# Performance work log

Hardware: AMD Instinct MI355X
Metric: run time of the kernel (lower is better)

## Reference

```python
import jax, jax.numpy as jnp
import numpy as np

B, S, D, H = 2, 2048, 1024, 16
DK = D // H


def setup_inputs() -> dict:
    key = jax.random.key(0)
    ks = jax.random.split(key, 11)
    sd = 1.0 / np.sqrt(D)  # torch Linear default init scale (uniform bound)
    def lin(k):
        kw, kb = jax.random.split(k)
        W = jax.random.uniform(kw, (D, D), jnp.float32, -sd, sd)
        b = jax.random.uniform(kb, (D,), jnp.float32, -sd, sd)
        return W, b
    Wq, bq = lin(ks[0]); Wk, bk = lin(ks[1]); Wv, bv = lin(ks[2]); Wo, bo = lin(ks[3])
    return {
        "Q": jax.random.normal(ks[4], (B, S, D), jnp.float32),
        "K": jax.random.normal(ks[5], (B, S, D), jnp.float32),
        "V": jax.random.normal(ks[6], (B, S, D), jnp.float32),
        "mask": jnp.ones((B, S), jnp.int32),
        "Wq": Wq, "bq": bq, "Wk": Wk, "bk": bk,
        "Wv": Wv, "bv": bv, "Wo": Wo, "bo": bo,
    }


def reference(Q, K, V, mask, Wq, bq, Wk, bk, Wv, bv, Wo, bo):
    b, s, _ = Q.shape
    # projections (torch Linear: x @ W.T + b), split heads -> [b, h, s, dk]
    def proj(x, W, bias):
        return (x @ W.T + bias).reshape(b, -1, H, DK).transpose(0, 2, 1, 3)
    q = proj(Q, Wq, bq)
    k = proj(K, Wk, bk)
    v = proj(V, Wv, bv)
    scores = jnp.einsum('bhqd,bhkd->bhqk', q, k) / jnp.sqrt(jnp.float32(DK))
    m = mask[:, None, None, :]  # [b,1,1,s_k]
    scores = jnp.where(m == 0, jnp.float32(-jnp.inf), scores)
    attn = jax.nn.softmax(scores, axis=-1)
    out = jnp.einsum('bhqk,bhkd->bhqd', attn, v)
    out = out.transpose(0, 2, 1, 3).reshape(b, s, H * DK)
    return out @ Wo.T + bo
```

## Files before the change

kernel.cpp:

```cpp
#include <hip/hip_runtime.h>
#include <stdint.h>

#define BB 2
#define HH 16
#define SS 2048
#define DKK 64
#define DD 1024
#define TT (BB * SS)

typedef __attribute__((ext_vector_type(8))) short bf16x8;
typedef __attribute__((ext_vector_type(4))) float f32x4;
typedef __attribute__((ext_vector_type(16))) float f32x16;

static __device__ __forceinline__ unsigned short f2bf(float f) {
  union { float f; uint32_t u; } c; c.f = f;
  return (unsigned short)((c.u + 0x7FFFu + ((c.u >> 16) & 1u)) >> 16);
}

static __device__ __forceinline__ f32x4 zero4() {
  f32x4 z; z[0] = 0.f; z[1] = 0.f; z[2] = 0.f; z[3] = 0.f; return z;
}
static __device__ __forceinline__ f32x16 zero16() {
  f32x16 z;
#pragma unroll
  for (int i = 0; i < 16; ++i) z[i] = 0.f;
  return z;
}

static __device__ __forceinline__ uint32_t cvt_pk_bf16(float lo, float hi) {
  uint32_t r;
  asm("v_cvt_pk_bf16_f32 %0, %1, %2" : "=v"(r) : "v"(lo), "v"(hi));
  return r;
}

static __device__ __forceinline__ uint32_t xswap_u32(uint32_t v) {
  return (uint32_t)__shfl_xor((int)v, 32);
}
static __device__ __forceinline__ float xhalf_sum(float x) {
  return x + __shfl_xor(x, 32);
}

static __device__ __forceinline__ void gload_lds16(const void* g, void* l) {
  __builtin_amdgcn_global_load_lds(
      (const __attribute__((address_space(1))) void*)g,
      (__attribute__((address_space(3))) void*)l, 16, 0, 0);
}

static __device__ __forceinline__ int swz(int row, int col) {
  return ((((col >> 3) ^ row) & 7) << 3) | (col & 7);
}

struct CvtArgs {
  const float* src[7];
  unsigned short* dst[7];
  int n4[7];
};

__global__ __launch_bounds__(256) void cvt_all(CvtArgs a) {
  const int id = blockIdx.y;
  const float4* s = (const float4*)a.src[id];
  ushort4* d = (ushort4*)a.dst[id];
  const int n4 = a.n4[id];
  for (int i = blockIdx.x * blockDim.x + threadIdx.x; i < n4;
       i += gridDim.x * blockDim.x) {
    float4 v = s[i];
    ushort4 o;
    o.x = f2bf(v.x); o.y = f2bf(v.y); o.z = f2bf(v.z); o.w = f2bf(v.w);
    d[i] = o;
  }
}

struct GemmJob {
  const unsigned short* A;
  const unsigned short* W;
  const float* bias;
  void* out;
  int mode;
  float scale;
};
struct GemmArgs { GemmJob job[3]; };

template <int BM, int NBUF>
__global__ __launch_bounds__(256) void gemm_kernel(GemmArgs args) {
  constexpr int MI = BM / 32;
  __shared__ __align__(16) unsigned short As[NBUF][BM][64];
  __shared__ __align__(16) unsigned short Bs[NBUF][128][64];
  const GemmJob jb = args.job[blockIdx.z];
  const int tid = threadIdx.x;
  const int lane = tid & 63;
  const int wv = tid >> 6;
  const int fr = lane & 15, fq = lane >> 4;
  const int wr = (wv >> 1) * (BM / 2), wc = (wv & 1) * 64;

  const int nb = gridDim.x * gridDim.y;
  const int bid = blockIdx.y * gridDim.x + blockIdx.x;
  const int virt = (bid & 7) * (nb >> 3) + (bid >> 3);
  const int n0 = (virt & 7) * 128, m0 = (virt >> 3) * BM;

  const int lrow = lane >> 3;
  const int lchunk = (lane & 7) ^ lrow;
  const unsigned short* __restrict__ A = jb.A;
  const unsigned short* __restrict__ W = jb.W;

  f32x4 acc[MI][4];
#pragma unroll
  for (int i = 0; i < MI; ++i)
#pragma unroll
    for (int j = 0; j < 4; ++j) acc[i][j] = zero4();

  constexpr int SEGA_W = BM / 32;
  constexpr int NT = DD / 64;

#define GSTAGE(buf, k0)                                                      \
  {                                                                          \
    _Pragma("unroll") for (int i = 0; i < SEGA_W; ++i) {                     \
      const int seg = wv * SEGA_W + i;                                       \
      const int row = seg * 8 + lrow;                                        \
      gload_lds16(A + (size_t)(m0 + row) * DD + (k0) + lchunk * 8,           \
                  (char*)&As[buf][0][0] + seg * 1024);                       \
    }                                                                        \
    _Pragma("unroll") for (int i = 0; i < 4; ++i) {                          \
      const int seg = wv * 4 + i;                                            \
      const int row = seg * 8 + lrow;                                        \
      gload_lds16(W + (size_t)(n0 + row) * DD + (k0) + lchunk * 8,           \
                  (char*)&Bs[buf][0][0] + seg * 1024);                       \
    }                                                                        \
  }

  int cur = 0;
  if (NBUF == 2) GSTAGE(0, 0);

  for (int t = 0; t < NT; ++t) {
    if (NBUF == 1) {
      __syncthreads();
      GSTAGE(0, t * 64);
      __syncthreads();
    } else {
      __syncthreads();
      if (t + 1 < NT) GSTAGE(cur ^ 1, (t + 1) * 64);
    }
#pragma unroll
    for (int kk = 0; kk < 2; ++kk) {
      bf16x8 af[MI], bfr[4];
#pragma unroll
      for (int i = 0; i < MI; ++i) {
        const int r = wr + i * 16 + fr;
        af[i] = *(const bf16x8*)&As[cur][r][swz(r, kk * 32 + fq * 8)];
      }
#pragma unroll
      for (int j = 0; j < 4; ++j) {
        const int r = wc + j * 16 + fr;
        bfr[j] = *(const bf16x8*)&Bs[cur][r][swz(r, kk * 32 + fq * 8)];
      }
      __builtin_amdgcn_s_setprio(1);
#pragma unroll
      for (int i = 0; i < MI; ++i)
#pragma unroll
        for (int j = 0; j < 4; ++j)
          acc[i][j] = __builtin_amdgcn_mfma_f32_16x16x32_bf16(af[i], bfr[j],
                                                              acc[i][j], 0, 0, 0);
      __builtin_amdgcn_s_setprio(0);
    }
    if (NBUF == 2) cur ^= 1;
  }
#undef GSTAGE

  const int mode = jb.mode;
  const float scale = jb.scale;
  if (mode == 1) {
    float* out = (float*)jb.out;
#pragma unroll
    for (int i = 0; i < MI; ++i)
#pragma unroll
      for (int j = 0; j < 4; ++j) {
        const int col = n0 + wc + j * 16 + fr;
        const float bv = jb.bias[col];
#pragma unroll
        for (int r = 0; r < 4; ++r) {
          const int row = m0 + wr + i * 16 + fq * 4 + r;
          out[(size_t)row * DD + col] = (acc[i][j][r] + bv) * scale;
        }
      }
  } else if (mode == 0) {
    unsigned short* out = (unsigned short*)jb.out;
#pragma unroll
    for (int i = 0; i < MI; ++i)
#pragma unroll
      for (int j = 0; j < 4; ++j) {
        const int col = n0 + wc + j * 16 + fr;
        const float bv = jb.bias[col];
        const int h = col >> 6, dk = col & 63;
#pragma unroll
        for (int r = 0; r < 4; ++r) {
          const int row = m0 + wr + i * 16 + fq * 4 + r;
          const int b = row >> 11, s = row & (SS - 1);
          out[(((size_t)(b * HH + h)) * SS + s) * DKK + dk] =
              f2bf((acc[i][j][r] + bv) * scale);
        }
      }
  } else {
    unsigned short* out = (unsigned short*)jb.out;
#pragma unroll
    for (int i = 0; i < MI; ++i)
#pragma unroll
      for (int j = 0; j < 4; ++j) {
        const int col = n0 + wc + j * 16 + fr;
        const float bv = jb.bias[col];
        const int h = col >> 6, dk = col & 63;
#pragma unroll
        for (int r = 0; r < 4; ++r) {
          const int row = m0 + wr + i * 16 + fq * 4 + r;
          const int b = row >> 11, s = row & (SS - 1);
          out[(((size_t)(b * HH + h)) * DKK + dk) * SS + s] =
              f2bf((acc[i][j][r] + bv) * scale);
        }
      }
  }
}

__global__ __launch_bounds__(512, 2) void attn_kernel(
    const unsigned short* __restrict__ qh, const unsigned short* __restrict__ kh,
    const unsigned short* __restrict__ vt, const int* __restrict__ maskp,
    unsigned short* __restrict__ ao) {
  __shared__ __align__(16) char smem[65536];

  const int tid = threadIdx.x;
  const int lane = tid & 63, wv = tid >> 6;
  const int lo = lane & 31, hi = lane >> 5;
  const int g = wv >> 2, qw = wv & 3;

  const int bid = blockIdx.x;
  const int virt = (bid & 7) * 32 + (bid >> 3);
  const int bh = virt >> 3, qblk = virt & 7;
  const int bB = bh >> 4, h = bh & 15;
  const int q0 = qblk * 256;
  const size_t base = (size_t)bh * SS * DKK;
  const size_t vbase = (size_t)bh * DKK * SS;

  const int lrow = lane >> 3;
  const int lchunk = (lane & 7) ^ lrow;
  const int srow = wv * 8 + lrow;

  bf16x8 aq[2][4];
#pragma unroll
  for (int st = 0; st < 2; ++st) {
    const int qrow = q0 + qw * 64 + st * 32 + lo;
#pragma unroll
    for (int tt = 0; tt < 4; ++tt)
      aq[st][tt] =
          *(const bf16x8*)(qh + base + (size_t)qrow * DKK + 16 * tt + hi * 8);
  }

  float lsum[2] = {0.f, 0.f};
  f32x16 o[2][2];
#pragma unroll
  for (int st = 0; st < 2; ++st) {
    o[st][0] = zero16();
    o[st][1] = zero16();
  }

  const int kvb = g * (SS / 2);
  constexpr int NTH = SS / 128;

  uint32_t okbits = 0;
  for (int t = 0; t < NTH; ++t) {
    const int mv = maskp[bB * SS + kvb + t * 64 + lane];
    okbits |= (__all(mv != 0)) ? (1u << t) : 0u;
  }

#define STAGE(d, t)                                                           \
  {                                                                           \
    const int ka = (t) * 64, kb2 = SS / 2 + (t) * 64;                         \
    gload_lds16(kh + base + (size_t)(ka + srow) * DKK + lchunk * 8,           \
                smem + ((d)) * 8192 + wv * 1024);                             \
    gload_lds16(vt + vbase + (size_t)srow * SS + ka + lchunk * 8,             \
                smem + 32768 + ((d)) * 8192 + wv * 1024);                     \
    gload_lds16(kh + base + (size_t)(kb2 + srow) * DKK + lchunk * 8,          \
                smem + (2 + (d)) * 8192 + wv * 1024);                         \
    gload_lds16(vt + vbase + (size_t)srow * SS + kb2 + lchunk * 8,            \
                smem + 32768 + (2 + (d)) * 8192 + wv * 1024);                 \
  }

  STAGE(0, 0);
  int cur = 0;

  for (int t = 0; t < NTH; ++t) {
    __syncthreads();
    if (t + 1 < NTH) STAGE(cur ^ 1, t + 1);
    const bool ok = (okbits >> t) & 1;

    const unsigned short* Ksb =
        (const unsigned short*)(smem + (g * 2 + cur) * 8192);
    const unsigned short* Vsb =
        (const unsigned short*)(smem + 32768 + (g * 2 + cur) * 8192);

    f32x16 sc[2][2];
#pragma unroll
    for (int st = 0; st < 2; ++st) { sc[st][0] = zero16(); sc[st][1] = zero16(); }
    __builtin_amdgcn_s_setprio(1);
#pragma unroll
    for (int tt = 0; tt < 4; ++tt) {
      bf16x8 k0 = *(const bf16x8*)&Ksb[lo * 64 + swz(lo, (hi + 2 * tt) * 8)];
      bf16x8 k1 =
          *(const bf16x8*)&Ksb[(32 + lo) * 64 + swz(32 + lo, (hi + 2 * tt) * 8)];
#pragma unroll
      for (int st = 0; st < 2; ++st) {
        sc[st][0] =
            __builtin_amdgcn_mfma_f32_32x32x16_bf16(k0, aq[st][tt], sc[st][0], 0, 0, 0);
        sc[st][1] =
            __builtin_amdgcn_mfma_f32_32x32x16_bf16(k1, aq[st][tt], sc[st][1], 0, 0, 0);
      }
    }
    __builtin_amdgcn_s_setprio(0);

    if (!ok) {
      const int mt = maskp[bB * SS + kvb + t * 64 + lane];
#pragma unroll
      for (int r = 0; r < 16; ++r) {
        const int kvi = (r & 3) + 8 * (r >> 2) + 4 * hi;
        const float a0 = (__shfl(mt, kvi) != 0) ? 0.f : -1e30f;
        const float a1 = (__shfl(mt, 32 + kvi) != 0) ? 0.f : -1e30f;
#pragma unroll
        for (int st = 0; st < 2; ++st) {
          sc[st][0][r] += a0;
          sc[st][1][r] += a1;
        }
      }
    }

    bf16x8 pb[2][4];
#pragma unroll
    for (int st = 0; st < 2; ++st) {
#pragma unroll
      for (int r = 0; r < 16; ++r) {
        sc[st][0][r] = __builtin_amdgcn_exp2f(sc[st][0][r]);
        sc[st][1][r] = __builtin_amdgcn_exp2f(sc[st][1][r]);
      }
      float t8[8];
#pragma unroll
      for (int i = 0; i < 8; ++i)
        t8[i] = (sc[st][0][2 * i] + sc[st][0][2 * i + 1]) +
                (sc[st][1][2 * i] + sc[st][1][2 * i + 1]);
      lsum[st] += ((t8[0] + t8[1]) + (t8[2] + t8[3])) +
                  ((t8[4] + t8[5]) + (t8[6] + t8[7]));

#pragma unroll
      for (int kb = 0; kb < 2; ++kb) {
#pragma unroll
        for (int tt = 0; tt < 2; ++tt) {
          const int b = tt * 8;
          uint32_t a0 = cvt_pk_bf16(sc[st][kb][b + 0], sc[st][kb][b + 1]);
          uint32_t a1 = cvt_pk_bf16(sc[st][kb][b + 2], sc[st][kb][b + 3]);
          uint32_t a2 = cvt_pk_bf16(sc[st][kb][b + 4], sc[st][kb][b + 5]);
          uint32_t a3 = cvt_pk_bf16(sc[st][kb][b + 6], sc[st][kb][b + 7]);
          const uint32_t e0 = xswap_u32(hi ? a0 : a2);
          const uint32_t e1 = xswap_u32(hi ? a1 : a3);
          union { uint32_t w[4]; bf16x8 v; } u;
          u.w[0] = hi ? e0 : a0;
          u.w[1] = hi ? e1 : a1;
          u.w[2] = hi ? a2 : e0;
          u.w[3] = hi ? a3 : e1;
          pb[st][kb * 2 + tt] = u.v;
        }
      }
    }

    __builtin_amdgcn_s_setprio(1);
#pragma unroll
    for (int tt = 0; tt < 4; ++tt) {
      bf16x8 v0 = *(const bf16x8*)&Vsb[lo * 64 + swz(lo, (hi + 2 * tt) * 8)];
      bf16x8 v1 =
          *(const bf16x8*)&Vsb[(32 + lo) * 64 + swz(32 + lo, (hi + 2 * tt) * 8)];
#pragma unroll
      for (int st = 0; st < 2; ++st) {
        o[st][0] = __builtin_amdgcn_mfma_f32_32x32x16_bf16(v0, pb[st][tt], o[st][0], 0, 0, 0);
        o[st][1] = __builtin_amdgcn_mfma_f32_32x32x16_bf16(v1, pb[st][tt], o[st][1], 0, 0, 0);
      }
    }
    __builtin_amdgcn_s_setprio(0);

    cur ^= 1;
  }
#undef STAGE

  lsum[0] = xhalf_sum(lsum[0]);
  lsum[1] = xhalf_sum(lsum[1]);

  float* mb = (float*)smem;
#pragma unroll
  for (int st = 0; st < 2; ++st) {
    const int rec = (qw * 64 + lane) * 33;
    __syncthreads();
    if (g == 1) {
      mb[rec] = lsum[st];
#pragma unroll
      for (int i = 0; i < 16; ++i) {
        mb[rec + 1 + i] = o[st][0][i];
        mb[rec + 17 + i] = o[st][1][i];
      }
    }
    __syncthreads();
    if (g == 0) {
      const float inv = 1.f / (lsum[st] + mb[rec]);
      const int token = bB * SS + q0 + qw * 64 + st * 32 + lo;
      unsigned short* aop = ao + (size_t)token * DD + h * DKK;
#pragma unroll
      for (int db = 0; db < 2; ++db) {
#pragma unroll
        for (int gq = 0; gq < 4; ++gq) {
          const int rb = rec + 1 + db * 16 + 4 * gq;
          float c0 = (o[st][db][4 * gq + 0] + mb[rb + 0]) * inv;
          float c1 = (o[st][db][4 * gq + 1] + mb[rb + 1]) * inv;
          float c2 = (o[st][db][4 * gq + 2] + mb[rb + 2]) * inv;
          float c3 = (o[st][db][4 * gq + 3] + mb[rb + 3]) * inv;
          uint2 w;
          w.x = cvt_pk_bf16(c0, c1);
          w.y = cvt_pk_bf16(c2, c3);
          *(uint2*)&aop[db * 32 + 8 * gq + 4 * hi] = w;
        }
      }
    }
  }
}

extern "C" void kernel_launch(void* const* d_in, const int* in_sizes, int n_in,
                              void* d_out, int out_size, void* d_ws, size_t ws_size,
                              hipStream_t stream) {
  const float* Q = (const float*)d_in[0];
  const float* K = (const float*)d_in[1];
  const float* V = (const float*)d_in[2];
  const int* mask = (const int*)d_in[3];
  const float* Wq = (const float*)d_in[4];
  const float* bq = (const float*)d_in[5];
  const float* Wk = (const float*)d_in[6];
  const float* bk = (const float*)d_in[7];
  const float* Wv = (const float*)d_in[8];
  const float* bv = (const float*)d_in[9];
  const float* Wo = (const float*)d_in[10];
  const float* bo = (const float*)d_in[11];

  char* ws = (char*)d_ws;
  const size_t SZ_X = (size_t)TT * DD * 2;
  const size_t SZ_W = (size_t)DD * DD * 2;
  unsigned short* Qb = (unsigned short*)(ws + 0 * SZ_X);
  unsigned short* Kb = (unsigned short*)(ws + 1 * SZ_X);
  unsigned short* Vb = (unsigned short*)(ws + 2 * SZ_X);
  unsigned short* Wqb = (unsigned short*)(ws + 3 * SZ_X);
  unsigned short* Wkb = (unsigned short*)(ws + 3 * SZ_X + 1 * SZ_W);
  unsigned short* Wvb = (unsigned short*)(ws + 3 * SZ_X + 2 * SZ_W);
  unsigned short* Wob = (unsigned short*)(ws + 3 * SZ_X + 3 * SZ_W);
  unsigned short* qh = (unsigned short*)(ws + 3 * SZ_X + 4 * SZ_W);
  unsigned short* kh = (unsigned short*)(ws + 4 * SZ_X + 4 * SZ_W);
  unsigned short* vt = (unsigned short*)(ws + 5 * SZ_X + 4 * SZ_W);
  unsigned short* ao = (unsigned short*)(ws + 6 * SZ_X + 4 * SZ_W);

  CvtArgs ca;
  ca.src[0] = Q;  ca.dst[0] = Qb;  ca.n4[0] = TT * DD / 4;
  ca.src[1] = K;  ca.dst[1] = Kb;  ca.n4[1] = TT * DD / 4;
  ca.src[2] = V;  ca.dst[2] = Vb;  ca.n4[2] = TT * DD / 4;
  ca.src[3] = Wq; ca.dst[3] = Wqb; ca.n4[3] = DD * DD / 4;
  ca.src[4] = Wk; ca.dst[4] = Wkb; ca.n4[4] = DD * DD / 4;
  ca.src[5] = Wv; ca.dst[5] = Wvb; ca.n4[5] = DD * DD / 4;
  ca.src[6] = Wo; ca.dst[6] = Wob; ca.n4[6] = DD * DD / 4;
  cvt_all<<<dim3(1024, 7), 256, 0, stream>>>(ca);

  const float SCALE_Q = 0.125f * 1.44269504088896f;

  GemmArgs ga;
  ga.job[0] = {Qb, Wqb, bq, qh, 0, SCALE_Q};
  ga.job[1] = {Kb, Wkb, bk, kh, 0, 1.0f};
  ga.job[2] = {Vb, Wvb, bv, vt, 2, 1.0f};
  gemm_kernel<64, 2><<<dim3(DD / 128, TT / 64, 3), 256, 0, stream>>>(ga);

  attn_kernel<<<dim3((TT / 256) * HH), 512, 0, stream>>>(qh, kh, vt, mask, ao);

  GemmArgs gf;
  gf.job[0] = {ao, Wob, bo, d_out, 1, 1.0f};
  gf.job[1] = gf.job[0];
  gf.job[2] = gf.job[0];
  gemm_kernel<64, 2><<<dim3(DD / 128, TT / 64, 1), 256, 0, stream>>>(gf);
}
```

Before: 113.5 us.

## Fuse fp32-to-bf16 activation conversion into QKV projection GEMM A-tile loads

The separate conversion pass for Q, K, V activations is removed; the QKV GEMM now reads fp32 activations directly, converts them to bf16 in registers and writes them to LDS, while weights are still pre-converted. This cuts the extra write and re-read of three bf16 activation copies (about 48MB of traffic) and shrinks the conversion kernel to weights only. In exchange, A-tile loads go through registers with synchronous global loads instead of async global-to-LDS copies, which may expose more latency in the GEMM main loop and doubles the A-side bytes read per tile.

```diff
diff --git a/kernel.cpp b/kernel.cpp
--- a/kernel.cpp
+++ b/kernel.cpp
@@ -51,9 +51,9 @@
 }
 
 struct CvtArgs {
-  const float* src[7];
-  unsigned short* dst[7];
-  int n4[7];
+  const float* src[4];
+  unsigned short* dst[4];
+  int n4[4];
 };
 
 __global__ __launch_bounds__(256) void cvt_all(CvtArgs a) {
@@ -71,7 +71,7 @@
 }
 
 struct GemmJob {
-  const unsigned short* A;
+  const void* A;
   const unsigned short* W;
   const float* bias;
   void* out;
@@ -80,7 +80,7 @@
 };
 struct GemmArgs { GemmJob job[3]; };
 
-template <int BM, int NBUF>
+template <int BM, int NBUF, bool AFP32>
 __global__ __launch_bounds__(256) void gemm_kernel(GemmArgs args) {
   constexpr int MI = BM / 32;
   __shared__ __align__(16) unsigned short As[NBUF][BM][64];
@@ -99,7 +99,8 @@
 
   const int lrow = lane >> 3;
   const int lchunk = (lane & 7) ^ lrow;
-  const unsigned short* __restrict__ A = jb.A;
+  const unsigned short* __restrict__ Ab = (const unsigned short*)jb.A;
+  const float* __restrict__ A32 = (const float*)jb.A;
   const unsigned short* __restrict__ W = jb.W;
 
   f32x4 acc[MI][4];
@@ -116,8 +117,20 @@
     _Pragma("unroll") for (int i = 0; i < SEGA_W; ++i) {                     \
       const int seg = wv * SEGA_W + i;                                       \
       const int row = seg * 8 + lrow;                                        \
-      gload_lds16(A + (size_t)(m0 + row) * DD + (k0) + lchunk * 8,           \
-                  (char*)&As[buf][0][0] + seg * 1024);                       \
+      if constexpr (AFP32) {                                                 \
+        const float* sp = A32 + (size_t)(m0 + row) * DD + (k0) + lchunk * 8; \
+        const float4 f0 = *(const float4*)sp;                                \
+        const float4 f1 = *(const float4*)(sp + 4);                          \
+        uint4 wdat;                                                          \
+        wdat.x = cvt_pk_bf16(f0.x, f0.y);                                    \
+        wdat.y = cvt_pk_bf16(f0.z, f0.w);                                    \
+        wdat.z = cvt_pk_bf16(f1.x, f1.y);                                    \
+        wdat.w = cvt_pk_bf16(f1.z, f1.w);                                    \
+        *(uint4*)((char*)&As[buf][0][0] + seg * 1024 + lane * 16) = wdat;    \
+      } else {                                                               \
+        gload_lds16(Ab + (size_t)(m0 + row) * DD + (k0) + lchunk * 8,        \
+                    (char*)&As[buf][0][0] + seg * 1024);                     \
+      }                                                                      \
     }                                                                        \
     _Pragma("unroll") for (int i = 0; i < 4; ++i) {                          \
       const int seg = wv * 4 + i;                                            \
@@ -128,17 +141,11 @@
   }
 
   int cur = 0;
-  if (NBUF == 2) GSTAGE(0, 0);
+  GSTAGE(0, 0);
 
   for (int t = 0; t < NT; ++t) {
-    if (NBUF == 1) {
-      __syncthreads();
-      GSTAGE(0, t * 64);
-      __syncthreads();
-    } else {
-      __syncthreads();
-      if (t + 1 < NT) GSTAGE(cur ^ 1, (t + 1) * 64);
-    }
+    __syncthreads();
+    if (t + 1 < NT) GSTAGE(cur ^ 1, (t + 1) * 64);
 #pragma unroll
     for (int kk = 0; kk < 2; ++kk) {
       bf16x8 af[MI], bfr[4];
@@ -161,7 +168,7 @@
                                                               acc[i][j], 0, 0, 0);
       __builtin_amdgcn_s_setprio(0);
     }
-    if (NBUF == 2) cur ^= 1;
+    cur ^= 1;
   }
 #undef GSTAGE
 
@@ -442,35 +449,29 @@
   char* ws = (char*)d_ws;
   const size_t SZ_X = (size_t)TT * DD * 2;
   const size_t SZ_W = (size_t)DD * DD * 2;
-  unsigned short* Qb = (unsigned short*)(ws + 0 * SZ_X);
-  unsigned short* Kb = (unsigned short*)(ws + 1 * SZ_X);
-  unsigned short* Vb = (unsigned short*)(ws + 2 * SZ_X);
-  unsigned short* Wqb = (unsigned short*)(ws + 3 * SZ_X);
-  unsigned short* Wkb = (unsigned short*)(ws + 3 * SZ_X + 1 * SZ_W);
-  unsigned short* Wvb = (unsigned short*)(ws + 3 * SZ_X + 2 * SZ_W);
-  unsigned short* Wob = (unsigned short*)(ws + 3 * SZ_X + 3 * SZ_W);
-  unsigned short* qh = (unsigned short*)(ws + 3 * SZ_X + 4 * SZ_W);
-  unsigned short* kh = (unsigned short*)(ws + 4 * SZ_X + 4 * SZ_W);
-  unsigned short* vt = (unsigned short*)(ws + 5 * SZ_X + 4 * SZ_W);
-  unsigned short* ao = (unsigned short*)(ws + 6 * SZ_X + 4 * SZ_W);
+  unsigned short* Wqb = (unsigned short*)(ws + 0 * SZ_W);
+  unsigned short* Wkb = (unsigned short*)(ws + 1 * SZ_W);
+  unsigned short* Wvb = (unsigned short*)(ws + 2 * SZ_W);
+  unsigned short* Wob = (unsigned short*)(ws + 3 * SZ_W);
+  unsigned short* qh = (unsigned short*)(ws + 4 * SZ_W + 0 * SZ_X);
+  unsigned short* kh = (unsigned short*)(ws + 4 * SZ_W + 1 * SZ_X);
+  unsigned short* vt = (unsigned short*)(ws + 4 * SZ_W + 2 * SZ_X);
+  unsigned short* ao = (unsigned short*)(ws + 4 * SZ_W + 3 * SZ_X);
 
   CvtArgs ca;
-  ca.src[0] = Q;  ca.dst[0] = Qb;  ca.n4[0] = TT * DD / 4;
-  ca.src[1] = K;  ca.dst[1] = Kb;  ca.n4[1] = TT * DD / 4;
-  ca.src[2] = V;  ca.dst[2] = Vb;  ca.n4[2] = TT * DD / 4;
-  ca.src[3] = Wq; ca.dst[3] = Wqb; ca.n4[3] = DD * DD / 4;
-  ca.src[4] = Wk; ca.dst[4] = Wkb; ca.n4[4] = DD * DD / 4;
-  ca.src[5] = Wv; ca.dst[5] = Wvb; ca.n4[5] = DD * DD / 4;
-  ca.src[6] = Wo; ca.dst[6] = Wob; ca.n4[6] = DD * DD / 4;
-  cvt_all<<<dim3(1024, 7), 256, 0, stream>>>(ca);
+  ca.src[0] = Wq; ca.dst[0] = Wqb; ca.n4[0] = DD * DD / 4;
+  ca.src[1] = Wk; ca.dst[1] = Wkb; ca.n4[1] = DD * DD / 4;
+  ca.src[2] = Wv; ca.dst[2] = Wvb; ca.n4[2] = DD * DD / 4;
+  ca.src[3] = Wo; ca.dst[3] = Wob; ca.n4[3] = DD * DD / 4;
+  cvt_all<<<dim3(512, 4), 256, 0, stream>>>(ca);
 
   const float SCALE_Q = 0.125f * 1.44269504088896f;
 
   GemmArgs ga;
-  ga.job[0] = {Qb, Wqb, bq, qh, 0, SCALE_Q};
-  ga.job[1] = {Kb, Wkb, bk, kh, 0, 1.0f};
-  ga.job[2] = {Vb, Wvb, bv, vt, 2, 1.0f};
-  gemm_kernel<64, 2><<<dim3(DD / 128, TT / 64, 3), 256, 0, stream>>>(ga);
+  ga.job[0] = {Q, Wqb, bq, qh, 0, SCALE_Q};
+  ga.job[1] = {K, Wkb, bk, kh, 0, 1.0f};
+  ga.job[2] = {V, Wvb, bv, vt, 2, 1.0f};
+  gemm_kernel<64, 2, true><<<dim3(DD / 128, TT / 64, 3), 256, 0, stream>>>(ga);
 
   attn_kernel<<<dim3((TT / 256) * HH), 512, 0, stream>>>(qh, kh, vt, mask, ao);
 
@@ -478,5 +479,5 @@
   gf.job[0] = {ao, Wob, bo, d_out, 1, 1.0f};
   gf.job[1] = gf.job[0];
   gf.job[2] = gf.job[0];
-  gemm_kernel<64, 2><<<dim3(DD / 128, TT / 64, 1), 256, 0, stream>>>(gf);
-}
+  gemm_kernel<64, 2, false><<<dim3(DD / 128, TT / 64, 1), 256, 0, stream>>>(gf);
+}
```

After: 113.0 us. About the same (-0.5%).

## Deepen attention K/V staging to four slots, one barrier per two tiles

Applied to the files above, without the earlier changes.

The attention kernel moves from a two-slot K/V ring with one barrier per 64-key tile to a four-slot ring in 128 KB of dynamic shared memory. Each barrier now prefetches two tiles ahead and computes two tiles, which halves the barrier count and gives loads more time to land. The cost is double the LDS per block, which can limit how many blocks fit on a CU, and it relies on large dynamic LDS being allowed at launch. The GEMM loses its unused single-buffer path as cleanup.

```diff
diff --git a/kernel.cpp b/kernel.cpp
--- a/kernel.cpp
+++ b/kernel.cpp
@@ -71,7 +71,7 @@
 }
 
 struct GemmJob {
-  const unsigned short* A;
+  const void* A;
   const unsigned short* W;
   const float* bias;
   void* out;
@@ -99,7 +99,7 @@
 
   const int lrow = lane >> 3;
   const int lchunk = (lane & 7) ^ lrow;
-  const unsigned short* __restrict__ A = jb.A;
+  const unsigned short* __restrict__ A = (const unsigned short*)jb.A;
   const unsigned short* __restrict__ W = jb.W;
 
   f32x4 acc[MI][4];
@@ -128,17 +128,11 @@
   }
 
   int cur = 0;
-  if (NBUF == 2) GSTAGE(0, 0);
+  GSTAGE(0, 0);
 
   for (int t = 0; t < NT; ++t) {
-    if (NBUF == 1) {
-      __syncthreads();
-      GSTAGE(0, t * 64);
-      __syncthreads();
-    } else {
-      __syncthreads();
-      if (t + 1 < NT) GSTAGE(cur ^ 1, (t + 1) * 64);
-    }
+    __syncthreads();
+    if (t + 1 < NT) GSTAGE(cur ^ 1, (t + 1) * 64);
 #pragma unroll
     for (int kk = 0; kk < 2; ++kk) {
       bf16x8 af[MI], bfr[4];
@@ -161,7 +155,7 @@
                                                               acc[i][j], 0, 0, 0);
       __builtin_amdgcn_s_setprio(0);
     }
-    if (NBUF == 2) cur ^= 1;
+    cur ^= 1;
   }
 #undef GSTAGE
 
@@ -222,7 +216,7 @@
     const unsigned short* __restrict__ qh, const unsigned short* __restrict__ kh,
     const unsigned short* __restrict__ vt, const int* __restrict__ maskp,
     unsigned short* __restrict__ ao) {
-  __shared__ __align__(16) char smem[65536];
+  extern __shared__ __align__(16) char smem[];
 
   const int tid = threadIdx.x;
   const int lane = tid & 63, wv = tid >> 6;
@@ -268,31 +262,27 @@
     okbits |= (__all(mv != 0)) ? (1u << t) : 0u;
   }
 
-#define STAGE(d, t)                                                           \
+#define STAGE_T(slot, t)                                                      \
   {                                                                           \
     const int ka = (t) * 64, kb2 = SS / 2 + (t) * 64;                         \
     gload_lds16(kh + base + (size_t)(ka + srow) * DKK + lchunk * 8,           \
-                smem + ((d)) * 8192 + wv * 1024);                             \
+                smem + (0 * 4 + (slot)) * 8192 + wv * 1024);                  \
+    gload_lds16(kh + base + (size_t)(kb2 + srow) * DKK + lchunk * 8,          \
+                smem + (1 * 4 + (slot)) * 8192 + wv * 1024);                  \
     gload_lds16(vt + vbase + (size_t)srow * SS + ka + lchunk * 8,             \
-                smem + 32768 + ((d)) * 8192 + wv * 1024);                     \
-    gload_lds16(kh + base + (size_t)(kb2 + srow) * DKK + lchunk * 8,          \
-                smem + (2 + (d)) * 8192 + wv * 1024);                         \
+                smem + 65536 + (0 * 4 + (slot)) * 8192 + wv * 1024);          \
     gload_lds16(vt + vbase + (size_t)srow * SS + kb2 + lchunk * 8,            \
-                smem + 32768 + (2 + (d)) * 8192 + wv * 1024);                 \
-  }
-
-  STAGE(0, 0);
-  int cur = 0;
-
-  for (int t = 0; t < NTH; ++t) {
-    __syncthreads();
-    if (t + 1 < NTH) STAGE(cur ^ 1, t + 1);
+                smem + 65536 + (1 * 4 + (slot)) * 8192 + wv * 1024);          \
+  }
+
+  bf16x8 pb[2][4];
+
+  auto compute_tile = [&](int t, int slot) {
     const bool ok = (okbits >> t) & 1;
-
     const unsigned short* Ksb =
-        (const unsigned short*)(smem + (g * 2 + cur) * 8192);
+        (const unsigned short*)(smem + (g * 4 + slot) * 8192);
     const unsigned short* Vsb =
-        (const unsigned short*)(smem + 32768 + (g * 2 + cur) * 8192);
+        (const unsigned short*)(smem + 65536 + (g * 4 + slot) * 8192);
 
     f32x16 sc[2][2];
 #pragma unroll
@@ -328,7 +318,6 @@
       }
     }
 
-    bf16x8 pb[2][4];
 #pragma unroll
     for (int st = 0; st < 2; ++st) {
 #pragma unroll
@@ -378,10 +367,22 @@
       }
     }
     __builtin_amdgcn_s_setprio(0);
-
-    cur ^= 1;
-  }
-#undef STAGE
+  };
+
+  STAGE_T(0, 0);
+  STAGE_T(1, 1);
+
+  constexpr int NP = NTH / 2;
+  for (int p = 0; p < NP; ++p) {
+    __syncthreads();
+    if (p + 1 < NP) {
+      STAGE_T((2 * p + 2) & 3, 2 * p + 2);
+      STAGE_T((2 * p + 3) & 3, 2 * p + 3);
+    }
+    compute_tile(2 * p, (2 * p) & 3);
+    compute_tile(2 * p + 1, (2 * p + 1) & 3);
+  }
+#undef STAGE_T
 
   lsum[0] = xhalf_sum(lsum[0]);
   lsum[1] = xhalf_sum(lsum[1]);
@@ -472,7 +473,7 @@
   ga.job[2] = {Vb, Wvb, bv, vt, 2, 1.0f};
   gemm_kernel<64, 2><<<dim3(DD / 128, TT / 64, 3), 256, 0, stream>>>(ga);
 
-  attn_kernel<<<dim3((TT / 256) * HH), 512, 0, stream>>>(qh, kh, vt, mask, ao);
+  attn_kernel<<<dim3((TT / 256) * HH), 512, 131072, stream>>>(qh, kh, vt, mask, ao);
 
   GemmArgs gf;
   gf.job[0] = {ao, Wob, bo, d_out, 1, 1.0f};
```

Result: slower. 128.0 us (+12.8%).
